# Performance work log

Hardware: AMD Instinct MI355X
Metric: run time of the kernel (lower is better)

Reference implementation:

```python
import jax, jax.numpy as jnp
import numpy as np
from jax import lax

INPUT_DIM = 3
HIDDEN_DIM = 256
SEQ_LEN = 262144


def setup_inputs() -> dict:
    key = jax.random.key(0)
    ks = jax.random.split(key, 8)
    s = 1.0 / np.sqrt(INPUT_DIM)
    sh = 1.0 / np.sqrt(HIDDEN_DIM)
    return {
        "u": jax.random.normal(ks[0], (INPUT_DIM, SEQ_LEN), dtype=jnp.float32),
        "dt": jnp.float32(1.0 / 3000.0),
        # RNODE params: dx = dt * tanh(A x + B u + bA)
        "A": jax.random.uniform(ks[1], (INPUT_DIM, INPUT_DIM), jnp.float32, -s, s),
        "B": jax.random.uniform(ks[2], (INPUT_DIM, INPUT_DIM), jnp.float32, -s, s),
        "bA": jax.random.uniform(ks[3], (INPUT_DIM,), jnp.float32, -s, s),
        # Linear_Model params: Linear(3,256) -> ReLU -> Linear(256,3)
        "W1": jax.random.uniform(ks[4], (HIDDEN_DIM, INPUT_DIM), jnp.float32, -s, s),
        "b1": jax.random.uniform(ks[5], (HIDDEN_DIM,), jnp.float32, -s, s),
        "W2": jax.random.uniform(ks[6], (INPUT_DIM, HIDDEN_DIM), jnp.float32, -sh, sh),
        "b2": jax.random.uniform(ks[7], (INPUT_DIM,), jnp.float32, -sh, sh),
    }


def reference(u, dt, A, B, bA, W1, b1, W2, b2):
    channels, seq_len = u.shape

    # Sequential ODE-RNN recurrence (Euler step): x_{t+1} = x_t + dt*tanh(A x + B u_t + bA)
    def step(x, u_t):
        x = x + dt * jnp.tanh(A @ x + B @ u_t + bA)
        return x, x

    x0 = jnp.zeros((channels,), dtype=u.dtype)
    _, xs = lax.scan(step, x0, u.T)          # xs: [S, C]
    membrane_potentials = xs.T               # [C, S]

    # Per-step feedforward MLP has no cross-time state -> apply vectorized over S.
    h = jax.nn.relu(jnp.einsum('hc,cs->hs', W1, membrane_potentials) + b1[:, None])
    outputs = jnp.einsum('ch,hs->cs', W2, h) + b2[:, None]  # [C, S]
    return outputs, membrane_potentials
```

## Files before the change

kernel.cpp:

```cpp
#include <hip/hip_runtime.h>

#define SEQ_LEN 262144
#define K 512
#define M 8
#define NG (SEQ_LEN / K)
#define NCORR 2
#define HID 256
#define C2LE 2.885390081777927f

template <int CTRL, int RM>
__device__ __forceinline__ float dpp_mov(float oldv, float v) {
    return __builtin_bit_cast(float, __builtin_amdgcn_update_dpp(
        __builtin_bit_cast(int, oldv), __builtin_bit_cast(int, v), CTRL, RM, 0xf, false));
}
template <int CTRL, int RM>
__device__ __forceinline__ float dpp_add(float v) {
    return v + dpp_mov<CTRL, RM>(0.0f, v);
}
__device__ __forceinline__ float wave_incl_scan(float v) {
    v = dpp_add<0x111, 0xf>(v);
    v = dpp_add<0x112, 0xf>(v);
    v = dpp_add<0x114, 0xf>(v);
    v = dpp_add<0x118, 0xf>(v);
    v = dpp_add<0x142, 0xa>(v);
    v = dpp_add<0x143, 0xc>(v);
    return v;
}
__device__ __forceinline__ float dpp_wshr1(float v) {
    return __builtin_bit_cast(float, __builtin_amdgcn_update_dpp(
        0, __builtin_bit_cast(int, v), 0x138, 0xf, 0xf, false));
}
__device__ __forceinline__ float readlane_f(float v, int lane) {
    return __builtin_bit_cast(
        float, __builtin_amdgcn_readlane(__builtin_bit_cast(int, v), lane));
}

struct Aff { float m[9]; float b[3]; };

__device__ __forceinline__ void compose(Aff& r, const Aff& n, const Aff& o) {
#pragma unroll
    for (int i = 0; i < 3; ++i) {
#pragma unroll
        for (int j = 0; j < 3; ++j)
            r.m[3*i+j] = fmaf(n.m[3*i+0], o.m[0+j],
                         fmaf(n.m[3*i+1], o.m[3+j],
                              n.m[3*i+2] * o.m[6+j]));
        r.b[i] = fmaf(n.m[3*i+0], o.b[0],
                 fmaf(n.m[3*i+1], o.b[1],
                 fmaf(n.m[3*i+2], o.b[2], n.b[i])));
    }
}

template <int CTRL, int RM>
__device__ __forceinline__ void scan_level(Aff& a) {
    Aff p;
    p.m[0] = dpp_mov<CTRL, RM>(1.f, a.m[0]);
    p.m[1] = dpp_mov<CTRL, RM>(0.f, a.m[1]);
    p.m[2] = dpp_mov<CTRL, RM>(0.f, a.m[2]);
    p.m[3] = dpp_mov<CTRL, RM>(0.f, a.m[3]);
    p.m[4] = dpp_mov<CTRL, RM>(1.f, a.m[4]);
    p.m[5] = dpp_mov<CTRL, RM>(0.f, a.m[5]);
    p.m[6] = dpp_mov<CTRL, RM>(0.f, a.m[6]);
    p.m[7] = dpp_mov<CTRL, RM>(0.f, a.m[7]);
    p.m[8] = dpp_mov<CTRL, RM>(1.f, a.m[8]);
    p.b[0] = dpp_mov<CTRL, RM>(0.f, a.b[0]);
    p.b[1] = dpp_mov<CTRL, RM>(0.f, a.b[1]);
    p.b[2] = dpp_mov<CTRL, RM>(0.f, a.b[2]);
    Aff r; compose(r, a, p); a = r;
}

template <int MODE>
__global__ __launch_bounds__(64) void shootk(
    const float* __restrict__ u,
    const float* __restrict__ Am,
    const float* __restrict__ dtp,
    const float* __restrict__ Bm,
    const float* __restrict__ bAp,
    const float4* __restrict__ jf_r,
    float4* __restrict__ jf_w,
    float4* __restrict__ xh,
    float* __restrict__ xs) {
    const int lane = threadIdx.x;
    const int g = blockIdx.x;
    const float dt = dtp[0];
    const float invdt3 = 1.0f / (3.0f * dt);
    float a[9], as[9];
#pragma unroll
    for (int i = 0; i < 9; ++i) { a[i] = Am[i]; as[i] = C2LE * Am[i]; }

    const int base = g * K + M * lane;
    float4 ua0 = *(const float4*)(u + base);
    float4 ua1 = *(const float4*)(u + base + 4);
    float4 ub0 = *(const float4*)(u + SEQ_LEN + base);
    float4 ub1 = *(const float4*)(u + SEQ_LEN + base + 4);
    float4 uc0 = *(const float4*)(u + 2 * SEQ_LEN + base);
    float4 uc1 = *(const float4*)(u + 2 * SEQ_LEN + base + 4);
    float B0 = Bm[0], B1 = Bm[1], B2 = Bm[2], B3 = Bm[3], B4 = Bm[4],
          B5 = Bm[5], B6 = Bm[6], B7 = Bm[7], B8 = Bm[8];
    float ba0 = bAp[0], ba1 = bAp[1], ba2 = bAp[2];
    float U0[M] = { ua0.x, ua0.y, ua0.z, ua0.w, ua1.x, ua1.y, ua1.z, ua1.w };
    float U1[M] = { ub0.x, ub0.y, ub0.z, ub0.w, ub1.x, ub1.y, ub1.z, ub1.w };
    float U2[M] = { uc0.x, uc0.y, uc0.z, uc0.w, uc1.x, uc1.y, uc1.z, uc1.w };
    float w0[M], w1[M], w2[M];
#pragma unroll
    for (int i = 0; i < M; ++i) {
        w0[i] = C2LE * fmaf(B0, U0[i], fmaf(B1, U1[i], fmaf(B2, U2[i], ba0)));
        w1[i] = C2LE * fmaf(B3, U0[i], fmaf(B4, U1[i], fmaf(B5, U2[i], ba1)));
        w2[i] = C2LE * fmaf(B6, U0[i], fmaf(B7, U1[i], fmaf(B8, U2[i], ba2)));
    }

    float x0 = 0.f, x1 = 0.f, x2 = 0.f;
    if (MODE != 0) {
        float J[8][9], dv[8][3], xhn0[8], xhn1[8], xhn2[8];
#pragma unroll
        for (int i = 0; i < 8; ++i) {
            int gg = 8 * lane + i;
            float4 q0v = jf_r[3*gg + 0], q1v = jf_r[3*gg + 1], q2v = jf_r[3*gg + 2];
            J[i][0] = q0v.x; J[i][1] = q0v.y; J[i][2] = q0v.z; J[i][3] = q0v.w;
            J[i][4] = q1v.x; J[i][5] = q1v.y; J[i][6] = q1v.z; J[i][7] = q1v.w;
            J[i][8] = q2v.x;
            float xn0 = 0.f, xn1 = 0.f, xn2 = 0.f;
            if (gg < NG - 1) {
                float4 xnv = xh[gg + 1];
                xn0 = xnv.x; xn1 = xnv.y; xn2 = xnv.z;
            }
            xhn0[i] = xn0; xhn1[i] = xn1; xhn2[i] = xn2;
            dv[i][0] = q2v.y - xn0;
            dv[i][1] = q2v.z - xn1;
            dv[i][2] = q2v.w - xn2;
        }
        Aff c;
#pragma unroll
        for (int k = 0; k < 9; ++k) c.m[k] = J[0][k];
        c.b[0] = dv[0][0]; c.b[1] = dv[0][1]; c.b[2] = dv[0][2];
#pragma unroll
        for (int i = 1; i < 8; ++i) {
            Aff s;
#pragma unroll
            for (int k = 0; k < 9; ++k) s.m[k] = J[i][k];
            s.b[0] = dv[i][0]; s.b[1] = dv[i][1]; s.b[2] = dv[i][2];
            Aff r; compose(r, s, c); c = r;
        }
        scan_level<0x111, 0xf>(c);
        scan_level<0x112, 0xf>(c);
        scan_level<0x114, 0xf>(c);
        scan_level<0x118, 0xf>(c);
        scan_level<0x142, 0xa>(c);
        scan_level<0x143, 0xc>(c);
        float ce0 = dpp_wshr1(c.b[0]);
        float ce1 = dpp_wshr1(c.b[1]);
        float ce2 = dpp_wshr1(c.b[2]);
#pragma unroll
        for (int i = 0; i < 8; ++i) {
            float n0 = fmaf(J[i][0], ce0, fmaf(J[i][1], ce1, fmaf(J[i][2], ce2, dv[i][0])));
            float n1 = fmaf(J[i][3], ce0, fmaf(J[i][4], ce1, fmaf(J[i][5], ce2, dv[i][1])));
            float n2 = fmaf(J[i][6], ce0, fmaf(J[i][7], ce1, fmaf(J[i][8], ce2, dv[i][2])));
            ce0 = n0; ce1 = n1; ce2 = n2;
            xhn0[i] += ce0; xhn1[i] += ce1; xhn2[i] += ce2;
        }
        if (g > 0) {
            const int tl = (g - 1) >> 3, idx = (g - 1) & 7;
            float p0 = xhn0[0], p1 = xhn1[0], p2 = xhn2[0];
#pragma unroll
            for (int i = 1; i < 8; ++i) {
                p0 = (idx == i) ? xhn0[i] : p0;
                p1 = (idx == i) ? xhn1[i] : p1;
                p2 = (idx == i) ? xhn2[i] : p2;
            }
            x0 = readlane_f(p0, tl);
            x1 = readlane_f(p1, tl);
            x2 = readlane_f(p2, tl);
        }
    }
    if (MODE != 2 && lane == 0) xh[g] = float4{ x0, x1, x2, 0.f };

    float zc0 = fmaf(as[0], x0, fmaf(as[1], x1, as[2] * x2));
    float zc1 = fmaf(as[3], x0, fmaf(as[4], x1, as[5] * x2));
    float zc2 = fmaf(as[6], x0, fmaf(as[7], x1, as[8] * x2));

    float t0s[M][3], c1s[M][3];
    Aff acc;
#pragma unroll
    for (int i = 0; i < M; ++i) {
        float z[3] = { w0[i] + zc0, w1[i] + zc1, w2[i] + zc2 };
        float cb[3], cv[3];
#pragma unroll
        for (int c = 0; c < 3; ++c) {
            float e  = __builtin_amdgcn_exp2f(z[c]);
            float r  = __builtin_amdgcn_rcpf(e + 1.0f);
            float t  = fmaf(-2.0f, r, 1.0f);
            float b  = dt * t;
            float c1 = fmaf(-b, t, dt);
            t0s[i][c] = t; c1s[i][c] = c1;
            cb[c] = b; cv[c] = c1;
        }
        Aff s;
        s.m[0] = fmaf(cv[0], a[0], 1.f); s.m[1] = cv[0] * a[1]; s.m[2] = cv[0] * a[2];
        s.m[3] = cv[1] * a[3]; s.m[4] = fmaf(cv[1], a[4], 1.f); s.m[5] = cv[1] * a[5];
        s.m[6] = cv[2] * a[6]; s.m[7] = cv[2] * a[7]; s.m[8] = fmaf(cv[2], a[8], 1.f);
        s.b[0] = cb[0]; s.b[1] = cb[1]; s.b[2] = cb[2];
        if (i == 0) acc = s;
        else { Aff r; compose(r, s, acc); acc = r; }
    }

    scan_level<0x111, 0xf>(acc);
    scan_level<0x112, 0xf>(acc);
    scan_level<0x114, 0xf>(acc);
    scan_level<0x118, 0xf>(acc);
    scan_level<0x142, 0xa>(acc);
    scan_level<0x143, 0xc>(acc);

    float ds0 = dpp_wshr1(acc.b[0]);
    float ds1 = dpp_wshr1(acc.b[1]);
    float ds2 = dpp_wshr1(acc.b[2]);

    float d0 = ds0, d1 = ds1, d2 = ds2;
    float outv[M][3];
#pragma unroll
    for (int i = 0; i < M; ++i) {
        float zz0 = fmaf(a[0], d0, fmaf(a[1], d1, a[2] * d2));
        float zz1 = fmaf(a[3], d0, fmaf(a[4], d1, a[5] * d2));
        float zz2 = fmaf(a[6], d0, fmaf(a[7], d1, a[8] * d2));
        float zz[3] = { zz0, zz1, zz2 };
        float dd[3];
#pragma unroll
        for (int c = 0; c < 3; ++c) {
            float t   = t0s[i][c], cv = c1s[i][c];
            float cb  = dt * t;
            float cT2 = -(t * cv);
            float pc  = fmaf(-invdt3, cv, 0.66666667f * (t * t));
            float cT3 = cv * pc;
            dd[c] = fmaf(fmaf(fmaf(cT3, zz[c], cT2), zz[c], cv), zz[c], cb);
        }
        d0 += dd[0]; d1 += dd[1]; d2 += dd[2];
        outv[i][0] = d0; outv[i][1] = d1; outv[i][2] = d2;
    }

    float q0 = d0 - acc.b[0], q1 = d1 - acc.b[1], q2 = d2 - acc.b[2];
    float e0 = wave_incl_scan(q0) - q0;
    float e1 = wave_incl_scan(q1) - q1;
    float e2 = wave_incl_scan(q2) - q2;
    float cor0 = x0 + e0, cor1 = x1 + e1, cor2 = x2 + e2;

    if (MODE == 2) {
        float4 s0a = { outv[0][0] + cor0, outv[1][0] + cor0, outv[2][0] + cor0, outv[3][0] + cor0 };
        float4 s0b = { outv[4][0] + cor0, outv[5][0] + cor0, outv[6][0] + cor0, outv[7][0] + cor0 };
        float4 s1a = { outv[0][1] + cor1, outv[1][1] + cor1, outv[2][1] + cor1, outv[3][1] + cor1 };
        float4 s1b = { outv[4][1] + cor1, outv[5][1] + cor1, outv[6][1] + cor1, outv[7][1] + cor1 };
        float4 s2a = { outv[0][2] + cor2, outv[1][2] + cor2, outv[2][2] + cor2, outv[3][2] + cor2 };
        float4 s2b = { outv[4][2] + cor2, outv[5][2] + cor2, outv[6][2] + cor2, outv[7][2] + cor2 };
        *(float4*)&xs[base]                   = s0a;
        *(float4*)&xs[base + 4]               = s0b;
        *(float4*)&xs[SEQ_LEN + base]         = s1a;
        *(float4*)&xs[SEQ_LEN + base + 4]     = s1b;
        *(float4*)&xs[2 * SEQ_LEN + base]     = s2a;
        *(float4*)&xs[2 * SEQ_LEN + base + 4] = s2b;
    } else {
        if (lane == 63) {
            float F0 = outv[M-1][0] + cor0;
            float F1 = outv[M-1][1] + cor1;
            float F2 = outv[M-1][2] + cor2;
            jf_w[3*g + 0] = float4{ acc.m[0], acc.m[1], acc.m[2], acc.m[3] };
            jf_w[3*g + 1] = float4{ acc.m[4], acc.m[5], acc.m[6], acc.m[7] };
            jf_w[3*g + 2] = float4{ acc.m[8], F0, F1, F2 };
        }
    }
}

__global__ __launch_bounds__(256) void mlp_kernel(
    const float* __restrict__ xs, const float* __restrict__ W1,
    const float* __restrict__ b1v, const float* __restrict__ W2,
    const float* __restrict__ b2v, float* __restrict__ out) {
    int s = blockIdx.x * 256 + threadIdx.x;
    float x0 = xs[s], x1 = xs[SEQ_LEN + s], x2 = xs[2 * SEQ_LEN + s];
    float acc0 = 0.f, acc1 = 0.f, acc2 = 0.f;
#pragma unroll 4
    for (int h = 0; h < HID; ++h) {
        float hv = fmaf(W1[3 * h + 0], x0,
                   fmaf(W1[3 * h + 1], x1,
                   fmaf(W1[3 * h + 2], x2, b1v[h])));
        hv = fmaxf(hv, 0.f);
        acc0 = fmaf(W2[h], hv, acc0);
        acc1 = fmaf(W2[HID + h], hv, acc1);
        acc2 = fmaf(W2[2 * HID + h], hv, acc2);
    }
    out[s] = acc0 + b2v[0];
    out[SEQ_LEN + s] = acc1 + b2v[1];
    out[2 * SEQ_LEN + s] = acc2 + b2v[2];
}

extern "C" void kernel_launch(void* const* d_in, const int* in_sizes, int n_in,
                              void* d_out, int out_size, void* d_ws, size_t ws_size,
                              hipStream_t stream) {
    const float* u  = (const float*)d_in[0];
    const float* dt = (const float*)d_in[1];
    const float* A  = (const float*)d_in[2];
    const float* B  = (const float*)d_in[3];
    const float* bA = (const float*)d_in[4];
    const float* W1 = (const float*)d_in[5];
    const float* b1 = (const float*)d_in[6];
    const float* W2 = (const float*)d_in[7];
    const float* b2 = (const float*)d_in[8];

    float* out  = (float*)d_out;
    float* memb = out + 3 * SEQ_LEN;

    float4* jfA = (float4*)d_ws;
    float4* jfB = jfA + 3 * NG;
    float4* xh  = jfB + 3 * NG;

    shootk<0><<<NG, 64, 0, stream>>>(u, A, dt, B, bA, nullptr, jfA, xh, nullptr);
    float4* rd = jfA;
    float4* wr = jfB;
    for (int j = 1; j < NCORR; ++j) {
        shootk<1><<<NG, 64, 0, stream>>>(u, A, dt, B, bA, rd, wr, xh, nullptr);
        float4* t = rd; rd = wr; wr = t;
    }
    shootk<2><<<NG, 64, 0, stream>>>(u, A, dt, B, bA, rd, nullptr, xh, memb);
    mlp_kernel<<<SEQ_LEN / 256, 256, 0, stream>>>(memb, W1, b1, W2, b2, out);
}
```

Baseline: 113.0 us.

## Fuse shooting passes and MLP into one cooperative kernel with grid syncs

Replaces the four separate launches (three shooting passes plus the MLP) with a single cooperative kernel of 512 blocks by 256 threads. Wave 0 runs the shooting phases separated by grid.sync, keeping per-lane state in registers across phases. The other three waves preload the MLP weights into LDS, and the trajectory is then staged in LDS for an in-block MLP. This is meant to remove launch gaps and the global round trip of the trajectory into the MLP. In exchange it adds grid-wide barrier cost and requires all blocks to be co-resident, with a fallback to the old launches if the cooperative launch fails.

```diff
diff --git a/kernel.cpp b/kernel.cpp
--- a/kernel.cpp
+++ b/kernel.cpp
@@ -1,10 +1,12 @@
 #include <hip/hip_runtime.h>
+#include <hip/hip_cooperative_groups.h>
+
+namespace cg = cooperative_groups;
 
 #define SEQ_LEN 262144
 #define K 512
 #define M 8
 #define NG (SEQ_LEN / K)
-#define NCORR 2
 #define HID 256
 #define C2LE 2.885390081777927f
 
@@ -70,15 +72,278 @@
 }
 
 template <int MODE>
-__global__ __launch_bounds__(64) void shootk(
+__device__ __forceinline__ void shoot_phase(
+    const int lane, const int g, const int base,
+    const float dt, const float invdt3,
+    const float (&a)[9], const float (&as)[9],
+    const float (&w0)[M], const float (&w1)[M], const float (&w2)[M],
+    const float4* __restrict__ jf_r, float4* __restrict__ jf_w,
+    float (&xk0)[8], float (&xk1)[8], float (&xk2)[8],
+    float* __restrict__ xs, float* lsx) {
+
+    float x0 = 0.f, x1 = 0.f, x2 = 0.f;
+    if (MODE != 0) {
+        float J[8][9], dv[8][3], xhn0[8], xhn1[8], xhn2[8];
+#pragma unroll
+        for (int i = 0; i < 8; ++i) {
+            int gg = 8 * lane + i;
+            float4 q0v = jf_r[3*gg + 0], q1v = jf_r[3*gg + 1], q2v = jf_r[3*gg + 2];
+            J[i][0] = q0v.x; J[i][1] = q0v.y; J[i][2] = q0v.z; J[i][3] = q0v.w;
+            J[i][4] = q1v.x; J[i][5] = q1v.y; J[i][6] = q1v.z; J[i][7] = q1v.w;
+            J[i][8] = q2v.x;
+            float xn0 = 0.f, xn1 = 0.f, xn2 = 0.f;
+            if (MODE == 2) { xn0 = xk0[i]; xn1 = xk1[i]; xn2 = xk2[i]; }
+            xhn0[i] = xn0; xhn1[i] = xn1; xhn2[i] = xn2;
+            dv[i][0] = q2v.y - xn0;
+            dv[i][1] = q2v.z - xn1;
+            dv[i][2] = q2v.w - xn2;
+        }
+        Aff c;
+#pragma unroll
+        for (int k = 0; k < 9; ++k) c.m[k] = J[0][k];
+        c.b[0] = dv[0][0]; c.b[1] = dv[0][1]; c.b[2] = dv[0][2];
+#pragma unroll
+        for (int i = 1; i < 8; ++i) {
+            Aff s;
+#pragma unroll
+            for (int k = 0; k < 9; ++k) s.m[k] = J[i][k];
+            s.b[0] = dv[i][0]; s.b[1] = dv[i][1]; s.b[2] = dv[i][2];
+            Aff r; compose(r, s, c); c = r;
+        }
+        scan_level<0x111, 0xf>(c);
+        scan_level<0x112, 0xf>(c);
+        scan_level<0x114, 0xf>(c);
+        scan_level<0x118, 0xf>(c);
+        scan_level<0x142, 0xa>(c);
+        scan_level<0x143, 0xc>(c);
+        float ce0 = dpp_wshr1(c.b[0]);
+        float ce1 = dpp_wshr1(c.b[1]);
+        float ce2 = dpp_wshr1(c.b[2]);
+#pragma unroll
+        for (int i = 0; i < 8; ++i) {
+            float n0 = fmaf(J[i][0], ce0, fmaf(J[i][1], ce1, fmaf(J[i][2], ce2, dv[i][0])));
+            float n1 = fmaf(J[i][3], ce0, fmaf(J[i][4], ce1, fmaf(J[i][5], ce2, dv[i][1])));
+            float n2 = fmaf(J[i][6], ce0, fmaf(J[i][7], ce1, fmaf(J[i][8], ce2, dv[i][2])));
+            ce0 = n0; ce1 = n1; ce2 = n2;
+            xhn0[i] += ce0; xhn1[i] += ce1; xhn2[i] += ce2;
+        }
+        if (MODE == 1) {
+#pragma unroll
+            for (int i = 0; i < 8; ++i) { xk0[i] = xhn0[i]; xk1[i] = xhn1[i]; xk2[i] = xhn2[i]; }
+        }
+        if (g > 0) {
+            const int tl = (g - 1) >> 3, idx = (g - 1) & 7;
+            float p0 = xhn0[0], p1 = xhn1[0], p2 = xhn2[0];
+#pragma unroll
+            for (int i = 1; i < 8; ++i) {
+                p0 = (idx == i) ? xhn0[i] : p0;
+                p1 = (idx == i) ? xhn1[i] : p1;
+                p2 = (idx == i) ? xhn2[i] : p2;
+            }
+            x0 = readlane_f(p0, tl);
+            x1 = readlane_f(p1, tl);
+            x2 = readlane_f(p2, tl);
+        }
+    }
+
+    float zc0 = fmaf(as[0], x0, fmaf(as[1], x1, as[2] * x2));
+    float zc1 = fmaf(as[3], x0, fmaf(as[4], x1, as[5] * x2));
+    float zc2 = fmaf(as[6], x0, fmaf(as[7], x1, as[8] * x2));
+
+    float t0s[M][3], c1s[M][3];
+    Aff acc;
+#pragma unroll
+    for (int i = 0; i < M; ++i) {
+        float z[3] = { w0[i] + zc0, w1[i] + zc1, w2[i] + zc2 };
+        float cb[3], cv[3];
+#pragma unroll
+        for (int c = 0; c < 3; ++c) {
+            float e  = __builtin_amdgcn_exp2f(z[c]);
+            float r  = __builtin_amdgcn_rcpf(e + 1.0f);
+            float t  = fmaf(-2.0f, r, 1.0f);
+            float b  = dt * t;
+            float c1 = fmaf(-b, t, dt);
+            t0s[i][c] = t; c1s[i][c] = c1;
+            cb[c] = b; cv[c] = c1;
+        }
+        Aff s;
+        s.m[0] = fmaf(cv[0], a[0], 1.f); s.m[1] = cv[0] * a[1]; s.m[2] = cv[0] * a[2];
+        s.m[3] = cv[1] * a[3]; s.m[4] = fmaf(cv[1], a[4], 1.f); s.m[5] = cv[1] * a[5];
+        s.m[6] = cv[2] * a[6]; s.m[7] = cv[2] * a[7]; s.m[8] = fmaf(cv[2], a[8], 1.f);
+        s.b[0] = cb[0]; s.b[1] = cb[1]; s.b[2] = cb[2];
+        if (i == 0) acc = s;
+        else { Aff r; compose(r, s, acc); acc = r; }
+    }
+
+    scan_level<0x111, 0xf>(acc);
+    scan_level<0x112, 0xf>(acc);
+    scan_level<0x114, 0xf>(acc);
+    scan_level<0x118, 0xf>(acc);
+    scan_level<0x142, 0xa>(acc);
+    scan_level<0x143, 0xc>(acc);
+
+    float ds0 = dpp_wshr1(acc.b[0]);
+    float ds1 = dpp_wshr1(acc.b[1]);
+    float ds2 = dpp_wshr1(acc.b[2]);
+
+    float d0 = ds0, d1 = ds1, d2 = ds2;
+    float outv[M][3];
+#pragma unroll
+    for (int i = 0; i < M; ++i) {
+        float zz0 = fmaf(a[0], d0, fmaf(a[1], d1, a[2] * d2));
+        float zz1 = fmaf(a[3], d0, fmaf(a[4], d1, a[5] * d2));
+        float zz2 = fmaf(a[6], d0, fmaf(a[7], d1, a[8] * d2));
+        float zz[3] = { zz0, zz1, zz2 };
+        float dd[3];
+#pragma unroll
+        for (int c = 0; c < 3; ++c) {
+            float t   = t0s[i][c], cv = c1s[i][c];
+            float cb  = dt * t;
+            float cT2 = -(t * cv);
+            float pc  = fmaf(-invdt3, cv, 0.66666667f * (t * t));
+            float cT3 = cv * pc;
+            dd[c] = fmaf(fmaf(fmaf(cT3, zz[c], cT2), zz[c], cv), zz[c], cb);
+        }
+        d0 += dd[0]; d1 += dd[1]; d2 += dd[2];
+        outv[i][0] = d0; outv[i][1] = d1; outv[i][2] = d2;
+    }
+
+    float q0 = d0 - acc.b[0], q1 = d1 - acc.b[1], q2 = d2 - acc.b[2];
+    float e0 = wave_incl_scan(q0) - q0;
+    float e1 = wave_incl_scan(q1) - q1;
+    float e2 = wave_incl_scan(q2) - q2;
+    float cor0 = x0 + e0, cor1 = x1 + e1, cor2 = x2 + e2;
+
+    if (MODE == 2) {
+        float4 s0a = { outv[0][0] + cor0, outv[1][0] + cor0, outv[2][0] + cor0, outv[3][0] + cor0 };
+        float4 s0b = { outv[4][0] + cor0, outv[5][0] + cor0, outv[6][0] + cor0, outv[7][0] + cor0 };
+        float4 s1a = { outv[0][1] + cor1, outv[1][1] + cor1, outv[2][1] + cor1, outv[3][1] + cor1 };
+        float4 s1b = { outv[4][1] + cor1, outv[5][1] + cor1, outv[6][1] + cor1, outv[7][1] + cor1 };
+        float4 s2a = { outv[0][2] + cor2, outv[1][2] + cor2, outv[2][2] + cor2, outv[3][2] + cor2 };
+        float4 s2b = { outv[4][2] + cor2, outv[5][2] + cor2, outv[6][2] + cor2, outv[7][2] + cor2 };
+        *(float4*)&xs[base]                   = s0a;
+        *(float4*)&xs[base + 4]               = s0b;
+        *(float4*)&xs[SEQ_LEN + base]         = s1a;
+        *(float4*)&xs[SEQ_LEN + base + 4]     = s1b;
+        *(float4*)&xs[2 * SEQ_LEN + base]     = s2a;
+        *(float4*)&xs[2 * SEQ_LEN + base + 4] = s2b;
+        const int li = M * lane;
+        *(float4*)&lsx[li]             = s0a; *(float4*)&lsx[li + 4]         = s0b;
+        *(float4*)&lsx[K + li]         = s1a; *(float4*)&lsx[K + li + 4]     = s1b;
+        *(float4*)&lsx[2 * K + li]     = s2a; *(float4*)&lsx[2 * K + li + 4] = s2b;
+    } else {
+        if (lane == 63) {
+            float F0 = outv[M-1][0] + cor0;
+            float F1 = outv[M-1][1] + cor1;
+            float F2 = outv[M-1][2] + cor2;
+            jf_w[3*g + 0] = float4{ acc.m[0], acc.m[1], acc.m[2], acc.m[3] };
+            jf_w[3*g + 1] = float4{ acc.m[4], acc.m[5], acc.m[6], acc.m[7] };
+            jf_w[3*g + 2] = float4{ acc.m[8], F0, F1, F2 };
+        }
+    }
+}
+
+__global__ __launch_bounds__(256, 2) void fused_kernel(
     const float* __restrict__ u,
     const float* __restrict__ Am,
     const float* __restrict__ dtp,
     const float* __restrict__ Bm,
     const float* __restrict__ bAp,
-    const float4* __restrict__ jf_r,
-    float4* __restrict__ jf_w,
-    float4* __restrict__ xh,
+    const float* __restrict__ W1,
+    const float* __restrict__ b1v,
+    const float* __restrict__ W2,
+    const float* __restrict__ b2v,
+    float4* __restrict__ jfA,
+    float4* __restrict__ jfB,
+    float* __restrict__ xs,
+    float* __restrict__ out) {
+    __shared__ float lsx[3 * K];
+    __shared__ float lw1[3 * HID], lb1[HID], lw2[3 * HID], lb2[3];
+
+    const int tid  = threadIdx.x;
+    const int lane = tid & 63;
+    const int wid  = tid >> 6;
+    const int g    = blockIdx.x;
+    const float dt = dtp[0];
+    const float invdt3 = 1.0f / (3.0f * dt);
+    const int base = g * K + M * lane;
+
+    cg::grid_group grid = cg::this_grid();
+
+    float a[9], as[9], w0[M], w1[M], w2[M];
+    float xk0[8], xk1[8], xk2[8];
+    if (wid == 0) {
+#pragma unroll
+        for (int i = 0; i < 9; ++i) { a[i] = Am[i]; as[i] = C2LE * Am[i]; }
+        float4 ua0 = *(const float4*)(u + base);
+        float4 ua1 = *(const float4*)(u + base + 4);
+        float4 ub0 = *(const float4*)(u + SEQ_LEN + base);
+        float4 ub1 = *(const float4*)(u + SEQ_LEN + base + 4);
+        float4 uc0 = *(const float4*)(u + 2 * SEQ_LEN + base);
+        float4 uc1 = *(const float4*)(u + 2 * SEQ_LEN + base + 4);
+        float B0 = Bm[0], B1 = Bm[1], B2 = Bm[2], B3 = Bm[3], B4 = Bm[4],
+              B5 = Bm[5], B6 = Bm[6], B7 = Bm[7], B8 = Bm[8];
+        float ba0 = bAp[0], ba1 = bAp[1], ba2 = bAp[2];
+        float U0[M] = { ua0.x, ua0.y, ua0.z, ua0.w, ua1.x, ua1.y, ua1.z, ua1.w };
+        float U1[M] = { ub0.x, ub0.y, ub0.z, ub0.w, ub1.x, ub1.y, ub1.z, ub1.w };
+        float U2[M] = { uc0.x, uc0.y, uc0.z, uc0.w, uc1.x, uc1.y, uc1.z, uc1.w };
+#pragma unroll
+        for (int i = 0; i < M; ++i) {
+            w0[i] = C2LE * fmaf(B0, U0[i], fmaf(B1, U1[i], fmaf(B2, U2[i], ba0)));
+            w1[i] = C2LE * fmaf(B3, U0[i], fmaf(B4, U1[i], fmaf(B5, U2[i], ba1)));
+            w2[i] = C2LE * fmaf(B6, U0[i], fmaf(B7, U1[i], fmaf(B8, U2[i], ba2)));
+        }
+        shoot_phase<0>(lane, g, base, dt, invdt3, a, as, w0, w1, w2,
+                       nullptr, jfA, xk0, xk1, xk2, nullptr, nullptr);
+    } else {
+        const int t = tid - 64;
+        for (int i = t; i < 3 * HID; i += 192) { lw1[i] = W1[i]; lw2[i] = W2[i]; }
+        for (int i = t; i < HID; i += 192) lb1[i] = b1v[i];
+        if (t < 3) lb2[t] = b2v[t];
+    }
+    __threadfence();
+    grid.sync();
+    __threadfence();
+    if (wid == 0)
+        shoot_phase<1>(lane, g, base, dt, invdt3, a, as, w0, w1, w2,
+                       jfA, jfB, xk0, xk1, xk2, nullptr, nullptr);
+    __threadfence();
+    grid.sync();
+    __threadfence();
+    if (wid == 0)
+        shoot_phase<2>(lane, g, base, dt, invdt3, a, as, w0, w1, w2,
+                       jfB, nullptr, xk0, xk1, xk2, xs, lsx);
+    __syncthreads();
+
+    float xa0 = lsx[tid],       xa1 = lsx[K + tid],       xa2 = lsx[2*K + tid];
+    float xb0 = lsx[256 + tid], xb1 = lsx[K + 256 + tid], xb2 = lsx[2*K + 256 + tid];
+    float A0 = 0.f, A1 = 0.f, A2 = 0.f, C0 = 0.f, C1 = 0.f, C2 = 0.f;
+#pragma unroll 4
+    for (int h = 0; h < HID; ++h) {
+        float p0 = lw1[3*h], p1 = lw1[3*h + 1], p2 = lw1[3*h + 2], bb = lb1[h];
+        float ha = fmaf(p0, xa0, fmaf(p1, xa1, fmaf(p2, xa2, bb)));
+        float hb = fmaf(p0, xb0, fmaf(p1, xb1, fmaf(p2, xb2, bb)));
+        ha = fmaxf(ha, 0.f); hb = fmaxf(hb, 0.f);
+        float q0 = lw2[h], q1 = lw2[HID + h], q2 = lw2[2*HID + h];
+        A0 = fmaf(q0, ha, A0); A1 = fmaf(q1, ha, A1); A2 = fmaf(q2, ha, A2);
+        C0 = fmaf(q0, hb, C0); C1 = fmaf(q1, hb, C1); C2 = fmaf(q2, hb, C2);
+    }
+    const float bb0 = lb2[0], bb1 = lb2[1], bb2 = lb2[2];
+    const int s = g * K + tid;
+    out[s]                     = A0 + bb0;
+    out[SEQ_LEN + s]           = A1 + bb1;
+    out[2*SEQ_LEN + s]         = A2 + bb2;
+    out[s + 256]               = C0 + bb0;
+    out[SEQ_LEN + s + 256]     = C1 + bb1;
+    out[2*SEQ_LEN + s + 256]   = C2 + bb2;
+}
+
+template <int MODE>
+__global__ __launch_bounds__(64) void shootk(
+    const float* __restrict__ u, const float* __restrict__ Am,
+    const float* __restrict__ dtp, const float* __restrict__ Bm,
+    const float* __restrict__ bAp, const float4* __restrict__ jf_r,
+    float4* __restrict__ jf_w, float4* __restrict__ xh,
     float* __restrict__ xs) {
     const int lane = threadIdx.x;
     const int g = blockIdx.x;
@@ -87,7 +352,6 @@
     float a[9], as[9];
 #pragma unroll
     for (int i = 0; i < 9; ++i) { a[i] = Am[i]; as[i] = C2LE * Am[i]; }
-
     const int base = g * K + M * lane;
     float4 ua0 = *(const float4*)(u + base);
     float4 ua1 = *(const float4*)(u + base + 4);
@@ -108,7 +372,6 @@
         w1[i] = C2LE * fmaf(B3, U0[i], fmaf(B4, U1[i], fmaf(B5, U2[i], ba1)));
         w2[i] = C2LE * fmaf(B6, U0[i], fmaf(B7, U1[i], fmaf(B8, U2[i], ba2)));
     }
-
     float x0 = 0.f, x1 = 0.f, x2 = 0.f;
     if (MODE != 0) {
         float J[8][9], dv[8][3], xhn0[8], xhn1[8], xhn2[8];
@@ -309,13 +572,16 @@
     float4* jfB = jfA + 3 * NG;
     float4* xh  = jfB + 3 * NG;
 
-    shootk<0><<<NG, 64, 0, stream>>>(u, A, dt, B, bA, nullptr, jfA, xh, nullptr);
-    float4* rd = jfA;
-    float4* wr = jfB;
-    for (int j = 1; j < NCORR; ++j) {
-        shootk<1><<<NG, 64, 0, stream>>>(u, A, dt, B, bA, rd, wr, xh, nullptr);
-        float4* t = rd; rd = wr; wr = t;
-    }
-    shootk<2><<<NG, 64, 0, stream>>>(u, A, dt, B, bA, rd, nullptr, xh, memb);
-    mlp_kernel<<<SEQ_LEN / 256, 256, 0, stream>>>(memb, W1, b1, W2, b2, out);
-}
+    void* args[] = { (void*)&u, (void*)&A, (void*)&dt, (void*)&B, (void*)&bA,
+                     (void*)&W1, (void*)&b1, (void*)&W2, (void*)&b2,
+                     (void*)&jfA, (void*)&jfB, (void*)&memb, (void*)&out };
+    hipError_t e = hipLaunchCooperativeKernel(
+        reinterpret_cast<const void*>(fused_kernel),
+        dim3(NG), dim3(256), args, 0, stream);
+    if (e != hipSuccess) {
+        shootk<0><<<NG, 64, 0, stream>>>(u, A, dt, B, bA, nullptr, jfA, xh, nullptr);
+        shootk<1><<<NG, 64, 0, stream>>>(u, A, dt, B, bA, jfA, jfB, xh, nullptr);
+        shootk<2><<<NG, 64, 0, stream>>>(u, A, dt, B, bA, jfB, nullptr, xh, memb);
+        mlp_kernel<<<SEQ_LEN / 256, 256, 0, stream>>>(memb, W1, b1, W2, b2, out);
+    }
+}
```

Result: slower. 334.7 us (+196.1%).

## Fuse three shooting launches into one persistent kernel with global barriers

Applied to the files above, without the earlier changes.

Merges the three shooting-pass kernels into a single launch of NG=512 single-wave blocks. The passes are separated by atomic-counter grid barriers, and the Jacobian/endpoint exchange uses coherent agent-scope loads and stores. The per-block correction state (xk) now stays in registers between phases, replacing the xh round-trip through global memory. This removes two kernel launch gaps and some global traffic, at the cost of spin-wait barriers, scalar coherent loads, and a memset launch. Correctness relies on all 512 blocks being co-resident.

```diff
diff --git a/kernel.cpp b/kernel.cpp
--- a/kernel.cpp
+++ b/kernel.cpp
@@ -4,7 +4,6 @@
 #define K 512
 #define M 8
 #define NG (SEQ_LEN / K)
-#define NCORR 2
 #define HID 256
 #define C2LE 2.885390081777927f
 
@@ -33,6 +32,22 @@
 __device__ __forceinline__ float readlane_f(float v, int lane) {
     return __builtin_bit_cast(
         float, __builtin_amdgcn_readlane(__builtin_bit_cast(int, v), lane));
+}
+
+__device__ __forceinline__ float coh_load(const float* p) {
+    return __hip_atomic_load(p, __ATOMIC_RELAXED, __HIP_MEMORY_SCOPE_AGENT);
+}
+__device__ __forceinline__ void coh_store(float* p, float v) {
+    __hip_atomic_store(p, v, __ATOMIC_RELAXED, __HIP_MEMORY_SCOPE_AGENT);
+}
+
+__device__ __forceinline__ void gbar(unsigned* ctr, unsigned target) {
+    asm volatile("s_waitcnt vmcnt(0) lgkmcnt(0)" ::: "memory");
+    if (threadIdx.x == 0)
+        __hip_atomic_fetch_add(ctr, 1u, __ATOMIC_RELAXED, __HIP_MEMORY_SCOPE_AGENT);
+    while (__hip_atomic_load(ctr, __ATOMIC_RELAXED, __HIP_MEMORY_SCOPE_AGENT) < target)
+        __builtin_amdgcn_s_sleep(2);
+    asm volatile("" ::: "memory");
 }
 
 struct Aff { float m[9]; float b[3]; };
@@ -70,44 +85,14 @@
 }
 
 template <int MODE>
-__global__ __launch_bounds__(64) void shootk(
-    const float* __restrict__ u,
-    const float* __restrict__ Am,
-    const float* __restrict__ dtp,
-    const float* __restrict__ Bm,
-    const float* __restrict__ bAp,
-    const float4* __restrict__ jf_r,
-    float4* __restrict__ jf_w,
-    float4* __restrict__ xh,
+__device__ __forceinline__ void shoot_phase(
+    const int lane, const int g, const int base,
+    const float dt, const float invdt3,
+    const float (&a)[9], const float (&as)[9],
+    const float (&w0)[M], const float (&w1)[M], const float (&w2)[M],
+    const float4* __restrict__ jf_r, float4* __restrict__ jf_w,
+    float (&xk0)[8], float (&xk1)[8], float (&xk2)[8],
     float* __restrict__ xs) {
-    const int lane = threadIdx.x;
-    const int g = blockIdx.x;
-    const float dt = dtp[0];
-    const float invdt3 = 1.0f / (3.0f * dt);
-    float a[9], as[9];
-#pragma unroll
-    for (int i = 0; i < 9; ++i) { a[i] = Am[i]; as[i] = C2LE * Am[i]; }
-
-    const int base = g * K + M * lane;
-    float4 ua0 = *(const float4*)(u + base);
-    float4 ua1 = *(const float4*)(u + base + 4);
-    float4 ub0 = *(const float4*)(u + SEQ_LEN + base);
-    float4 ub1 = *(const float4*)(u + SEQ_LEN + base + 4);
-    float4 uc0 = *(const float4*)(u + 2 * SEQ_LEN + base);
-    float4 uc1 = *(const float4*)(u + 2 * SEQ_LEN + base + 4);
-    float B0 = Bm[0], B1 = Bm[1], B2 = Bm[2], B3 = Bm[3], B4 = Bm[4],
-          B5 = Bm[5], B6 = Bm[6], B7 = Bm[7], B8 = Bm[8];
-    float ba0 = bAp[0], ba1 = bAp[1], ba2 = bAp[2];
-    float U0[M] = { ua0.x, ua0.y, ua0.z, ua0.w, ua1.x, ua1.y, ua1.z, ua1.w };
-    float U1[M] = { ub0.x, ub0.y, ub0.z, ub0.w, ub1.x, ub1.y, ub1.z, ub1.w };
-    float U2[M] = { uc0.x, uc0.y, uc0.z, uc0.w, uc1.x, uc1.y, uc1.z, uc1.w };
-    float w0[M], w1[M], w2[M];
-#pragma unroll
-    for (int i = 0; i < M; ++i) {
-        w0[i] = C2LE * fmaf(B0, U0[i], fmaf(B1, U1[i], fmaf(B2, U2[i], ba0)));
-        w1[i] = C2LE * fmaf(B3, U0[i], fmaf(B4, U1[i], fmaf(B5, U2[i], ba1)));
-        w2[i] = C2LE * fmaf(B6, U0[i], fmaf(B7, U1[i], fmaf(B8, U2[i], ba2)));
-    }
 
     float x0 = 0.f, x1 = 0.f, x2 = 0.f;
     if (MODE != 0) {
@@ -115,19 +100,19 @@
 #pragma unroll
         for (int i = 0; i < 8; ++i) {
             int gg = 8 * lane + i;
-            float4 q0v = jf_r[3*gg + 0], q1v = jf_r[3*gg + 1], q2v = jf_r[3*gg + 2];
-            J[i][0] = q0v.x; J[i][1] = q0v.y; J[i][2] = q0v.z; J[i][3] = q0v.w;
-            J[i][4] = q1v.x; J[i][5] = q1v.y; J[i][6] = q1v.z; J[i][7] = q1v.w;
-            J[i][8] = q2v.x;
+            const float* src = (const float*)(jf_r + 3 * gg);
+            float Jv[12];
+#pragma unroll
+            for (int k = 0; k < 12; ++k) Jv[k] = coh_load(src + k);
+            J[i][0] = Jv[0]; J[i][1] = Jv[1]; J[i][2] = Jv[2];
+            J[i][3] = Jv[3]; J[i][4] = Jv[4]; J[i][5] = Jv[5];
+            J[i][6] = Jv[6]; J[i][7] = Jv[7]; J[i][8] = Jv[8];
             float xn0 = 0.f, xn1 = 0.f, xn2 = 0.f;
-            if (gg < NG - 1) {
-                float4 xnv = xh[gg + 1];
-                xn0 = xnv.x; xn1 = xnv.y; xn2 = xnv.z;
-            }
+            if (MODE == 2) { xn0 = xk0[i]; xn1 = xk1[i]; xn2 = xk2[i]; }
             xhn0[i] = xn0; xhn1[i] = xn1; xhn2[i] = xn2;
-            dv[i][0] = q2v.y - xn0;
-            dv[i][1] = q2v.z - xn1;
-            dv[i][2] = q2v.w - xn2;
+            dv[i][0] = Jv[9]  - xn0;
+            dv[i][1] = Jv[10] - xn1;
+            dv[i][2] = Jv[11] - xn2;
         }
         Aff c;
 #pragma unroll
@@ -158,6 +143,10 @@
             ce0 = n0; ce1 = n1; ce2 = n2;
             xhn0[i] += ce0; xhn1[i] += ce1; xhn2[i] += ce2;
         }
+        if (MODE == 1) {
+#pragma unroll
+            for (int i = 0; i < 8; ++i) { xk0[i] = xhn0[i]; xk1[i] = xhn1[i]; xk2[i] = xhn2[i]; }
+        }
         if (g > 0) {
             const int tl = (g - 1) >> 3, idx = (g - 1) & 7;
             float p0 = xhn0[0], p1 = xhn1[0], p2 = xhn2[0];
@@ -172,7 +161,6 @@
             x2 = readlane_f(p2, tl);
         }
     }
-    if (MODE != 2 && lane == 0) xh[g] = float4{ x0, x1, x2, 0.f };
 
     float zc0 = fmaf(as[0], x0, fmaf(as[1], x1, as[2] * x2));
     float zc1 = fmaf(as[3], x0, fmaf(as[4], x1, as[5] * x2));
@@ -257,14 +245,66 @@
         *(float4*)&xs[2 * SEQ_LEN + base + 4] = s2b;
     } else {
         if (lane == 63) {
-            float F0 = outv[M-1][0] + cor0;
-            float F1 = outv[M-1][1] + cor1;
-            float F2 = outv[M-1][2] + cor2;
-            jf_w[3*g + 0] = float4{ acc.m[0], acc.m[1], acc.m[2], acc.m[3] };
-            jf_w[3*g + 1] = float4{ acc.m[4], acc.m[5], acc.m[6], acc.m[7] };
-            jf_w[3*g + 2] = float4{ acc.m[8], F0, F1, F2 };
-        }
-    }
+            float vals[12] = { acc.m[0], acc.m[1], acc.m[2], acc.m[3], acc.m[4],
+                               acc.m[5], acc.m[6], acc.m[7], acc.m[8],
+                               outv[M-1][0] + cor0, outv[M-1][1] + cor1,
+                               outv[M-1][2] + cor2 };
+            float* dst = (float*)(jf_w + 3 * g);
+#pragma unroll
+            for (int k = 0; k < 12; ++k) coh_store(dst + k, vals[k]);
+        }
+    }
+}
+
+__global__ __launch_bounds__(64) void shoot_fused(
+    const float* __restrict__ u,
+    const float* __restrict__ Am,
+    const float* __restrict__ dtp,
+    const float* __restrict__ Bm,
+    const float* __restrict__ bAp,
+    float4* __restrict__ jfA,
+    float4* __restrict__ jfB,
+    unsigned* __restrict__ ctr,
+    float* __restrict__ xs) {
+    const int lane = threadIdx.x;
+    const int g = blockIdx.x;
+    const float dt = dtp[0];
+    const float invdt3 = 1.0f / (3.0f * dt);
+    const int base = g * K + M * lane;
+
+    float a[9], as[9];
+#pragma unroll
+    for (int i = 0; i < 9; ++i) { a[i] = Am[i]; as[i] = C2LE * Am[i]; }
+
+    float4 ua0 = *(const float4*)(u + base);
+    float4 ua1 = *(const float4*)(u + base + 4);
+    float4 ub0 = *(const float4*)(u + SEQ_LEN + base);
+    float4 ub1 = *(const float4*)(u + SEQ_LEN + base + 4);
+    float4 uc0 = *(const float4*)(u + 2 * SEQ_LEN + base);
+    float4 uc1 = *(const float4*)(u + 2 * SEQ_LEN + base + 4);
+    float B0 = Bm[0], B1 = Bm[1], B2 = Bm[2], B3 = Bm[3], B4 = Bm[4],
+          B5 = Bm[5], B6 = Bm[6], B7 = Bm[7], B8 = Bm[8];
+    float ba0 = bAp[0], ba1 = bAp[1], ba2 = bAp[2];
+    float U0[M] = { ua0.x, ua0.y, ua0.z, ua0.w, ua1.x, ua1.y, ua1.z, ua1.w };
+    float U1[M] = { ub0.x, ub0.y, ub0.z, ub0.w, ub1.x, ub1.y, ub1.z, ub1.w };
+    float U2[M] = { uc0.x, uc0.y, uc0.z, uc0.w, uc1.x, uc1.y, uc1.z, uc1.w };
+    float w0[M], w1[M], w2[M];
+#pragma unroll
+    for (int i = 0; i < M; ++i) {
+        w0[i] = C2LE * fmaf(B0, U0[i], fmaf(B1, U1[i], fmaf(B2, U2[i], ba0)));
+        w1[i] = C2LE * fmaf(B3, U0[i], fmaf(B4, U1[i], fmaf(B5, U2[i], ba1)));
+        w2[i] = C2LE * fmaf(B6, U0[i], fmaf(B7, U1[i], fmaf(B8, U2[i], ba2)));
+    }
+
+    float xk0[8], xk1[8], xk2[8];
+    shoot_phase<0>(lane, g, base, dt, invdt3, a, as, w0, w1, w2,
+                   nullptr, jfA, xk0, xk1, xk2, nullptr);
+    gbar(ctr, NG);
+    shoot_phase<1>(lane, g, base, dt, invdt3, a, as, w0, w1, w2,
+                   jfA, jfB, xk0, xk1, xk2, nullptr);
+    gbar(ctr, 2 * NG);
+    shoot_phase<2>(lane, g, base, dt, invdt3, a, as, w0, w1, w2,
+                   jfB, nullptr, xk0, xk1, xk2, xs);
 }
 
 __global__ __launch_bounds__(256) void mlp_kernel(
@@ -307,15 +347,10 @@
 
     float4* jfA = (float4*)d_ws;
     float4* jfB = jfA + 3 * NG;
-    float4* xh  = jfB + 3 * NG;
-
-    shootk<0><<<NG, 64, 0, stream>>>(u, A, dt, B, bA, nullptr, jfA, xh, nullptr);
-    float4* rd = jfA;
-    float4* wr = jfB;
-    for (int j = 1; j < NCORR; ++j) {
-        shootk<1><<<NG, 64, 0, stream>>>(u, A, dt, B, bA, rd, wr, xh, nullptr);
-        float4* t = rd; rd = wr; wr = t;
-    }
-    shootk<2><<<NG, 64, 0, stream>>>(u, A, dt, B, bA, rd, nullptr, xh, memb);
+    unsigned* ctr = (unsigned*)(jfB + 3 * NG);
+
+    hipMemsetAsync(ctr, 0, 64, stream);
+
+    shoot_fused<<<NG, 64, 0, stream>>>(u, A, dt, B, bA, jfA, jfB, ctr, memb);
     mlp_kernel<<<SEQ_LEN / 256, 256, 0, stream>>>(memb, W1, b1, W2, b2, out);
 }
```

Measured after the change: 160.5 us. 42.0% more time.
